# Kernel tuning notes

Hardware: AMD Instinct MI355X
Metric: run time of the kernel (lower is better)

## Reference

```python
import jax, jax.numpy as jnp
import numpy as np

Q_DIM, T_DIM, TOP_M, TEMP = 512, 768, 5, 0.07
B, H, W, K = 8, 64, 64, 128
LN_EPS = 1e-5

def _layernorm(x, g, b):
    mu = jnp.mean(x, axis=-1, keepdims=True)
    var = jnp.mean(jnp.square(x - mu), axis=-1, keepdims=True)
    return (x - mu) * jax.lax.rsqrt(var + LN_EPS) * g + b

def _l2norm(x):
    n = jnp.linalg.norm(x, axis=-1, keepdims=True)
    return x / jnp.maximum(n, 1e-12)

def setup_inputs() -> dict:
    key = jax.random.key(0)
    ks = jax.random.split(key, 12)
    s = lambda d: 1.0 / np.sqrt(d)
    return {
        'visual_features': jax.random.normal(ks[0], (B, H, W, Q_DIM), jnp.float32),
        'text_features': jax.random.normal(ks[1], (B, K, T_DIM), jnp.float32),
        'Wq': jax.random.uniform(ks[2], (Q_DIM, T_DIM), jnp.float32, -s(Q_DIM), s(Q_DIM)),
        'bq': jnp.zeros((T_DIM,), jnp.float32),
        'Wv': jax.random.uniform(ks[3], (T_DIM, Q_DIM), jnp.float32, -s(T_DIM), s(T_DIM)),
        'bv': jnp.zeros((Q_DIM,), jnp.float32),
        'W1': jax.random.uniform(ks[4], (Q_DIM, 4 * Q_DIM), jnp.float32, -s(Q_DIM), s(Q_DIM)),
        'b1': jnp.zeros((4 * Q_DIM,), jnp.float32),
        'W2': jax.random.uniform(ks[5], (4 * Q_DIM, Q_DIM), jnp.float32, -s(4 * Q_DIM), s(4 * Q_DIM)),
        'b2': jnp.zeros((Q_DIM,), jnp.float32),
        'g1': jnp.ones((Q_DIM,), jnp.float32), 'be1': jnp.zeros((Q_DIM,), jnp.float32),
        'g2': jnp.ones((Q_DIM,), jnp.float32), 'be2': jnp.zeros((Q_DIM,), jnp.float32),
    }

def reference(visual_features, text_features, Wq, bq, Wv, bv, W1, b1, W2, b2, g1, be1, g2, be2):
    b, h, w, c = visual_features.shape
    residual = visual_features.reshape(b, h * w, c)
    vis = _layernorm(residual, g1, be1)                      # (B,N,C)
    query = _l2norm(vis @ Wq + bq)                            # (B,N,Ct)
    keyt = _l2norm(text_features)                             # (B,K,Ct)
    value = text_features @ Wv + bv                           # (B,K,C)
    sim = jnp.einsum('bnc,bkc->bnk', query, keyt)             # (B,N,K)
    # top-M sparsification: keep top_m logits, others -> -inf
    top_v = jax.lax.top_k(sim, TOP_M)[0]                      # (B,N,M) sorted desc
    thr = top_v[..., -1:]
    sim = jnp.where(sim >= thr, sim, -jnp.inf)
    attn = jax.nn.softmax(sim / TEMP, axis=-1)
    aligned = jnp.einsum('bnk,bkc->bnc', attn, value)
    fused = residual + aligned
    fused = _layernorm(fused, g2, be2)
    ffn = jax.nn.gelu(fused @ W1 + b1, approximate=False) @ W2 + b2
    out = fused + ffn
    return out.reshape(b, h, w, c)
```

## Files before the change

kernel.cpp:

```cpp
#include <hip/hip_runtime.h>
#include <math.h>

typedef unsigned short u16;
typedef unsigned int   u32;
typedef unsigned long long u64;
typedef __attribute__((ext_vector_type(4))) float f32x4;
typedef __attribute__((ext_vector_type(4))) unsigned int u32x4;
typedef __attribute__((ext_vector_type(8))) _Float16 f16x8;
typedef __attribute__((ext_vector_type(8))) short s16x8;

#define NROWS   32768
#define CDIM    512
#define TDIM    768
#define KKEY    128
#define FFDIM   2048
#define NB      8
#define RPB     4096
#define LN_EPS_ 1e-5f
#define TINV    (1.0f/0.07f)
#define RESCUE_MARGIN 1e-5f

__device__ __forceinline__ u16 f2h(float f){ _Float16 h=(_Float16)f; return __builtin_bit_cast(u16,h); }
__device__ __forceinline__ float h2f(u16 v){ return (float)__builtin_bit_cast(_Float16, v); }
__device__ __forceinline__ unsigned pk2(float a,float b){ return (unsigned)f2h(a)|((unsigned)f2h(b)<<16); }
__device__ __forceinline__ u16 f2b(float f){
  u32 u = __builtin_bit_cast(u32, f);
  u32 r = (u + 0x7fffu + ((u>>16)&1u)) >> 16;
  return (u16)r;
}
__device__ __forceinline__ float b2f(u16 h){ u32 u = ((u32)h)<<16; return __builtin_bit_cast(float, u); }
__device__ __forceinline__ unsigned pkb(float a,float b){ return (unsigned)f2b(a)|((unsigned)f2b(b)<<16); }

__device__ __forceinline__ void gl_lds16(const void* g, void* l){
  __builtin_amdgcn_global_load_lds(
      (const __attribute__((address_space(1))) u32*)g,
      (__attribute__((address_space(3))) u32*)l, 16, 0, 0);
}

__device__ __forceinline__ float fast_exp2(float x){
#if __has_builtin(__builtin_amdgcn_exp2f)
  return __builtin_amdgcn_exp2f(x);
#else
  return exp2f(x);
#endif
}
__device__ __forceinline__ float fast_rcp(float x){
#if __has_builtin(__builtin_amdgcn_rcpf)
  return __builtin_amdgcn_rcpf(x);
#else
  return 1.0f/x;
#endif
}

__device__ __forceinline__ float wsumf(float v){
#pragma unroll
  for(int o=1;o<64;o<<=1) v+=__shfl_xor(v,o);
  return v; }
__device__ __forceinline__ float wmaxf(float v){
#pragma unroll
  for(int o=1;o<64;o<<=1) v=fmaxf(v,__shfl_xor(v,o));
  return v; }
__device__ __forceinline__ double wsumd(double v){
#pragma unroll
  for(int o=1;o<64;o<<=1) v+=__shfl_xor(v,o);
  return v; }
__device__ __forceinline__ double wmaxd(double v){
#pragma unroll
  for(int o=1;o<64;o<<=1){ double t=__shfl_xor(v,o); v = t>v ? t : v; }
  return v; }

__device__ __forceinline__ double blocksumd4(double v, double* red){
  const int lane = threadIdx.x & 63, w = threadIdx.x >> 6;
  v = wsumd(v);
  __syncthreads();
  if (lane==0) red[w] = v;
  __syncthreads();
  return red[0]+red[1]+red[2]+red[3];
}

template<int R, int C, int MODE>
__device__ __forceinline__ void tr_tile(const float* __restrict__ in, void* __restrict__ out,
                                        int bx, int by, float (*tile)[33])
{
  int c0 = bx*32, r0 = by*32;
  int tx = threadIdx.x, ty = threadIdx.y;
#pragma unroll
  for (int i=0;i<4;i++){
    int r = r0 + ty + i*8;
    tile[ty+i*8][tx] = in[(size_t)r*C + c0 + tx];
  }
  __syncthreads();
#pragma unroll
  for (int i=0;i<4;i++){
    int cc = c0 + ty + i*8, rr = r0 + tx;
    float v = tile[tx][ty+i*8];
    if (MODE==1)      ((u16*)out)[(size_t)cc*R + rr] = f2h(v);
    else if (MODE==2) ((u16*)out)[(size_t)cc*R + rr] = f2b(v);
    else              ((float*)out)[(size_t)cc*R + rr] = v;
  }
}

__global__ __launch_bounds__(256) void transpose_all_kernel(
    const float* __restrict__ Wq, const float* __restrict__ W1,
    const float* __restrict__ W2, const float* __restrict__ Wv,
    u16* __restrict__ Wqbt, u16* __restrict__ W116t,
    u16* __restrict__ W216t, float* __restrict__ WvT)
{
  __shared__ float tile[32][33];
  int bid = blockIdx.x;
  if (bid < 384){
    tr_tile<512,768,2>(Wq, Wqbt, bid%24, bid/24, tile);
  } else if (bid < 1408){
    int b = bid-384;  tr_tile<512,2048,1>(W1, W116t, b%64, b/64, tile);
  } else if (bid < 2432){
    int b = bid-1408; tr_tile<2048,512,1>(W2, W216t, b%16, b/16, tile);
  } else {
    int b = bid-2432; tr_tile<768,512,0>(Wv, WvT, b%16, b/16, tile);
  }
}

__global__ __launch_bounds__(256) void keystats_kernel(
    const float* __restrict__ text, const float* __restrict__ bq,
    float* __restrict__ normk, float* __restrict__ crr)
{
  int gw = blockIdx.x*4 + (threadIdx.x>>6);
  int lane = threadIdx.x & 63;
  const float* tr = &text[(size_t)gw*TDIM];
  double ss=0.0, db=0.0;
#pragma unroll
  for (int i=0;i<12;i++){
    float v = tr[lane + 64*i];
    ss += (double)v*(double)v;
    db += (double)bq[lane+64*i]*(double)v;
  }
  ss = wsumd(ss); db = wsumd(db);
  if (lane==0){
    double nk = sqrt(ss); nk = nk>1e-12 ? nk : 1e-12;
    normk[gw] = (float)nk;
    crr[gw]   = (float)db;
  }
}

__global__ __launch_bounds__(256) void ln1_kernel(
    const float* __restrict__ visual, const float* __restrict__ g1, const float* __restrict__ be1,
    u16* __restrict__ visH, u16* __restrict__ visL)
{
  int row = blockIdx.x*4 + (threadIdx.x>>6);
  int lane = threadIdx.x & 63;
  size_t base = (size_t)row*CDIM + lane*8;
  f32x4 a = *(const f32x4*)&visual[base];
  f32x4 c = *(const f32x4*)&visual[base+4];
  float s = a[0]+a[1]+a[2]+a[3]+c[0]+c[1]+c[2]+c[3];
  s = wsumf(s);
  float mu = s * (1.0f/512.0f);
  float q = 0.f;
#pragma unroll
  for (int i=0;i<4;i++){ float d=a[i]-mu; q+=d*d; }
#pragma unroll
  for (int i=0;i<4;i++){ float d=c[i]-mu; q+=d*d; }
  q = wsumf(q);
  float rs = rsqrtf(q*(1.0f/512.0f) + LN_EPS_);
  int cb = lane*8;
  float o[8];
#pragma unroll
  for (int i=0;i<4;i++) o[i]   = (a[i]-mu)*rs*g1[cb+i]   + be1[cb+i];
#pragma unroll
  for (int i=0;i<4;i++) o[4+i] = (c[i]-mu)*rs*g1[cb+4+i] + be1[cb+4+i];
  u16 hh[8];
  float lo[8];
#pragma unroll
  for (int i=0;i<8;i++){ hh[i] = f2b(o[i]); lo[i] = o[i] - b2f(hh[i]); }
  u32x4 hv, lv;
#pragma unroll
  for (int i=0;i<4;i++){
    hv[i] = (u32)hh[2*i] | ((u32)hh[2*i+1]<<16);
    lv[i] = pkb(lo[2*i], lo[2*i+1]);
  }
  *(u32x4*)&visH[base] = hv;
  *(u32x4*)&visL[base] = lv;
}

__global__ __launch_bounds__(256) void gemm_txt_kernel(
    const float* __restrict__ text, const float* __restrict__ Wq,
    const float* __restrict__ WvT,
    u16* __restrict__ MrtH, u16* __restrict__ MrtL, float* __restrict__ value)
{
  __shared__ float As[64][17];
  __shared__ float Bs[64][17];
  const int zz = blockIdx.z;
  const bool isV = zz >= 8;
  const int z = isV ? zz-8 : zz;
  const float* A  = text + (size_t)z*KKEY*TDIM;
  const float* Bt = isV ? WvT : Wq;
  const int tid = threadIdx.x;
  const int tx = tid & 15, ty = tid >> 4;
  const int m0 = blockIdx.x*64, n0 = blockIdx.y*64;
  float acc[4][4];
#pragma unroll
  for (int i=0;i<4;i++)
#pragma unroll
    for (int j=0;j<4;j++) acc[i][j]=0.f;
  const int lr = tid >> 2, lc = (tid & 3)*4;
  for (int k0=0; k0<TDIM; k0+=16){
    f32x4 av = *(const f32x4*)&A [(size_t)(m0+lr)*TDIM + k0 + lc];
    f32x4 bv = *(const f32x4*)&Bt[(size_t)(n0+lr)*TDIM + k0 + lc];
#pragma unroll
    for (int i=0;i<4;i++){ As[lr][lc+i]=av[i]; Bs[lr][lc+i]=bv[i]; }
    __syncthreads();
#pragma unroll
    for (int kk=0; kk<16; kk++){
      float a[4], b[4];
#pragma unroll
      for (int i=0;i<4;i++){ a[i]=As[ty*4+i][kk]; b[i]=Bs[tx*4+i][kk]; }
#pragma unroll
      for (int i=0;i<4;i++)
#pragma unroll
        for (int j=0;j<4;j++) acc[i][j] = fmaf(a[i], b[j], acc[i][j]);
    }
    __syncthreads();
  }
#pragma unroll
  for (int i=0;i<4;i++){
    size_t idx = ((size_t)z*KKEY + m0 + ty*4 + i)*CDIM + n0 + tx*4;
    if (isV){
      f32x4 o;
#pragma unroll
      for (int j=0;j<4;j++) o[j]=acc[i][j];
      *(f32x4*)&value[idx] = o;
    } else {
      u16 hh[4]; u16 ll[4];
#pragma unroll
      for (int j=0;j<4;j++){
        float v = acc[i][j];
        u16 h = f2b(v);
        hh[j] = h;
        ll[j] = f2b(v - b2f(h));
      }
      ((u32*)&MrtH[idx])[0] = (u32)hh[0] | ((u32)hh[1]<<16);
      ((u32*)&MrtH[idx])[1] = (u32)hh[2] | ((u32)hh[3]<<16);
      ((u32*)&MrtL[idx])[0] = (u32)ll[0] | ((u32)ll[1]<<16);
      ((u32*)&MrtL[idx])[1] = (u32)ll[2] | ((u32)ll[3]<<16);
    }
  }
}

__device__ __forceinline__ float gelu_exact(float v){
  float x  = v*0.70710678118654752440f;
  float ax = fabsf(x);
  float t  = fast_rcp(fmaf(0.3275911f, ax, 1.0f));
  float p  = t*fmaf(t, fmaf(t, fmaf(t, fmaf(t, 1.061405429f, -1.453152027f),
                  1.421413741f), -0.284496736f), 0.254829592f);
  float e  = fast_exp2(ax*ax*(-1.4426950408889634f));
  float y  = 1.0f - p*e;
  float er = (x < 0.0f) ? -y : y;
  return 0.5f*v*(1.0f + er);
}

template<int EPI, int NN, int KK, int NT, int TPB>
__global__ __launch_bounds__(256) void gemm_f16_kernel(
    const u16* __restrict__ A, const u16* __restrict__ Bt,
    const float* __restrict__ bias,
    float* __restrict__ out_f,
    u16* __restrict__ out_h,
    const u16* __restrict__ add_h)
{
  __shared__ __align__(16) u16 As[2][128*64];
  __shared__ __align__(16) u16 Bs[2][128*64];
  constexpr int KSTEPS = KK/64;
  constexpr int BPM = NT/TPB;
  constexpr int NWG = 256*BPM;
  constexpr int GTOT = TPB*KSTEPS;
  const int tid = threadIdx.x;
  const int lane = tid & 63, w = tid >> 6;
  const int wr = w >> 1, wc = w & 1;
  const int wg = blockIdx.x;
  const int b2 = (wg & 7)*(NWG/8) + (wg >> 3);
  const int mtile = b2 / BPM, nb = (b2 % BPM)*TPB;
  const int m0 = mtile*128;
  f32x4 acc[4][4];
#pragma unroll
  for (int i=0;i<4;i++)
#pragma unroll
    for (int j=0;j<4;j++) acc[i][j] = (f32x4)0.f;
  const int lr = lane & 15, lk = (lane >> 4)*8;
  const int c8_sw = ((lane & 7) ^ (lane >> 3))*8;
  const size_t stride32 = (size_t)32*KK;
  const int rowoff = w*8 + (lane>>3);
  const u16* aBase = &A [(size_t)(m0 + rowoff)*KK + c8_sw];
  const u16* bBase = &Bt[(size_t)(nb*128 + rowoff)*KK + c8_sw];

  auto STAGE = [&](int g, int buf){
    const int t = g / KSTEPS, k0 = (g & (KSTEPS-1))*64;
    const u16* ap = aBase + k0;
    const u16* bp = bBase + (size_t)t*128*KK + k0;
#pragma unroll
    for (int i=0;i<4;i++){
      gl_lds16(ap + i*stride32, &As[buf][w*512 + i*2048]);
      gl_lds16(bp + i*stride32, &Bs[buf][w*512 + i*2048]);
    }
  };

  const int lr4 = (lane >> 4)*4;
  STAGE(0, 0);
  for (int g=0; g<GTOT; ++g){
    const int cur = g & 1;
    if (g+1 < GTOT){
      STAGE(g+1, cur^1);
      asm volatile("s_waitcnt vmcnt(8)" ::: "memory");
    } else {
      asm volatile("s_waitcnt vmcnt(0)" ::: "memory");
    }
    __builtin_amdgcn_s_barrier();
#pragma unroll
    for (int kk=0; kk<64; kk+=32){
      s16x8 af[4], bfv[4];
      const int csw = (kk + lk) ^ ((lr & 7) << 3);
#pragma unroll
      for (int mi=0;mi<4;mi++) af[mi]  = *(const s16x8*)&As[cur][(wr*64 + mi*16 + lr)*64 + csw];
#pragma unroll
      for (int ni=0;ni<4;ni++) bfv[ni] = *(const s16x8*)&Bs[cur][(wc*64 + ni*16 + lr)*64 + csw];
#pragma unroll
      for (int mi=0;mi<4;mi++)
#pragma unroll
        for (int ni=0;ni<4;ni++){
          if (EPI == 0)
            acc[mi][ni] = __builtin_amdgcn_mfma_f32_16x16x32_bf16(af[mi], bfv[ni], acc[mi][ni], 0, 0, 0);
          else
            acc[mi][ni] = __builtin_amdgcn_mfma_f32_16x16x32_f16(
                __builtin_bit_cast(f16x8, af[mi]), __builtin_bit_cast(f16x8, bfv[ni]), acc[mi][ni], 0, 0, 0);
        }
    }
    __builtin_amdgcn_s_barrier();
    if ((g & (KSTEPS-1)) == KSTEPS-1){
      const int ntile = nb + g/KSTEPS;
      const int n0 = ntile*128;
      if (EPI == 0){
        float sq[4][4];
#pragma unroll
        for (int mi=0;mi<4;mi++)
#pragma unroll
          for (int r=0;r<4;r++) sq[mi][r]=0.f;
#pragma unroll
        for (int ni=0;ni<4;ni++){
          float bqv = bias[n0 + wc*64 + ni*16 + lr];
#pragma unroll
          for (int mi=0;mi<4;mi++)
#pragma unroll
            for (int r=0;r<4;r++){
              float v = acc[mi][ni][r] + bqv;
              sq[mi][r] += v*v;
            }
        }
#pragma unroll
        for (int o=1;o<16;o<<=1)
#pragma unroll
          for (int mi=0;mi<4;mi++)
#pragma unroll
            for (int r=0;r<4;r++) sq[mi][r] += __shfl_xor(sq[mi][r], o);
        if ((lane & 15) == 0){
          int part = ntile*2 + wc;
#pragma unroll
          for (int mi=0;mi<4;mi++)
#pragma unroll
            for (int r=0;r<4;r++){
              int row = m0 + wr*64 + mi*16 + lr4 + r;
              out_f[(size_t)row*12 + part] = sq[mi][r];
            }
        }
      } else {
        const int row0 = m0 + wr*64 + lr4;
        const int col0 = n0 + wc*64 + lr;
        float bb[4];
#pragma unroll
        for (int ni=0;ni<4;ni++) bb[ni] = bias[col0 + ni*16];
        if (EPI == 1){
          u16* op = out_h + (size_t)row0*NN + col0;
#pragma unroll
          for (int mi=0;mi<4;mi++)
#pragma unroll
            for (int r=0;r<4;r++)
#pragma unroll
              for (int ni=0;ni<4;ni++)
                op[(size_t)(mi*16+r)*NN + ni*16] = f2h(gelu_exact(acc[mi][ni][r] + bb[ni]));
        } else {
          float* op = out_f + (size_t)row0*NN + col0;
          const u16* rp = add_h + (size_t)row0*NN + col0;
#pragma unroll
          for (int mi=0;mi<4;mi++)
#pragma unroll
            for (int r=0;r<4;r++)
#pragma unroll
              for (int ni=0;ni<4;ni++)
                op[(size_t)(mi*16+r)*NN + ni*16] =
                    acc[mi][ni][r] + bb[ni] + h2f(rp[(size_t)(mi*16+r)*NN + ni*16]);
        }
      }
#pragma unroll
      for (int i=0;i<4;i++)
#pragma unroll
        for (int j=0;j<4;j++) acc[i][j] = (f32x4)0.f;
    }
  }
}

__global__ __launch_bounds__(256) void gemm_t_kernel(
    const u16* __restrict__ Ah, const u16* __restrict__ Al,
    const u16* __restrict__ Bh, const u16* __restrict__ Bl,
    float* __restrict__ C)
{
  __shared__ __align__(16) u16 As[2][128*64];
  __shared__ __align__(16) u16 Bs[2][128*64];
  const int tid = threadIdx.x;
  const int lane = tid & 63, w = tid >> 6;
  const int wr = w >> 1, wc = w & 1;
  const int wg = blockIdx.x;
  const int mtile = (wg & 7)*32 + (wg >> 3);
  const int m0 = mtile*128, z = mtile >> 5;
  f32x4 acc[4][4];
#pragma unroll
  for (int i=0;i<4;i++)
#pragma unroll
    for (int j=0;j<4;j++) acc[i][j] = (f32x4)0.f;
  const int lr = lane & 15, lk = (lane >> 4)*8;
  const int c8_sw = ((lane & 7) ^ (lane >> 3))*8;
  const int rowoff = w*8 + (lane>>3);
  const size_t aOff = (size_t)(m0 + rowoff)*CDIM + c8_sw;
  const size_t bOff = (size_t)(z*KKEY + rowoff)*CDIM + c8_sw;
  const size_t stride32 = (size_t)32*CDIM;

  auto STAGE = [&](int g, int buf){
    const int p = g >> 3, k0 = (g & 7) << 6;
    const u16* Ap = (p==2) ? Al : Ah;
    const u16* Bp = (p==1) ? Bl : Bh;
#pragma unroll
    for (int i=0;i<4;i++){
      gl_lds16(Ap + aOff + i*stride32 + k0, &As[buf][w*512 + i*2048]);
      gl_lds16(Bp + bOff + i*stride32 + k0, &Bs[buf][w*512 + i*2048]);
    }
  };

  STAGE(0, 0);
  for (int g=0; g<24; ++g){
    const int cur = g & 1;
    if (g < 23){
      STAGE(g+1, cur^1);
      asm volatile("s_waitcnt vmcnt(8)" ::: "memory");
    } else {
      asm volatile("s_waitcnt vmcnt(0)" ::: "memory");
    }
    __builtin_amdgcn_s_barrier();
#pragma unroll
    for (int kk=0; kk<64; kk+=32){
      s16x8 af[4], bfv[4];
      const int csw = (kk + lk) ^ ((lr & 7) << 3);
#pragma unroll
      for (int mi=0;mi<4;mi++) af[mi]  = *(const s16x8*)&As[cur][(wr*64 + mi*16 + lr)*64 + csw];
#pragma unroll
      for (int ni=0;ni<4;ni++) bfv[ni] = *(const s16x8*)&Bs[cur][(wc*64 + ni*16 + lr)*64 + csw];
#pragma unroll
      for (int mi=0;mi<4;mi++)
#pragma unroll
        for (int ni=0;ni<4;ni++)
          acc[mi][ni] = __builtin_amdgcn_mfma_f32_16x16x32_bf16(af[mi], bfv[ni], acc[mi][ni], 0, 0, 0);
    }
    __builtin_amdgcn_s_barrier();
  }
  const int lr4 = (lane >> 4)*4;
  const int row0 = m0 + wr*64 + lr4;
  const int col0 = wc*64 + lr;
  float* op = C + (size_t)row0*KKEY + col0;
#pragma unroll
  for (int mi=0;mi<4;mi++)
#pragma unroll
    for (int r=0;r<4;r++)
#pragma unroll
      for (int ni=0;ni<4;ni++)
        op[(size_t)(mi*16+r)*KKEY + ni*16] = acc[mi][ni][r];
}

__global__ __launch_bounds__(256) void rescue_kernel(
    const int* __restrict__ rcnt, const int* __restrict__ rlist,
    const float* __restrict__ visual, const float* __restrict__ text,
    const float* __restrict__ Wq, const float* __restrict__ bq,
    const float* __restrict__ g1, const float* __restrict__ be1,
    const float* __restrict__ g2, const float* __restrict__ be2,
    const float* __restrict__ value, const float* __restrict__ bv,
    u16* __restrict__ fused16)
{
  __shared__ double vis64[512];
  __shared__ double q64[768];
  __shared__ double sims[128];
  __shared__ double pw[128];
  __shared__ double red[4];
  __shared__ double sc2[2];
  __shared__ int klist[128];
  __shared__ int kcount;
  const int tid = threadIdx.x, lane = tid & 63, w = tid >> 6;
  int n = *rcnt; if (n > NROWS) n = NROWS;
  for (int i = blockIdx.x; i < n; i += gridDim.x){
    const int row = rlist[i], b = row >> 12;
    const size_t rb = (size_t)row*CDIM;
    double x0 = (double)visual[rb+tid], x1 = (double)visual[rb+tid+256];
    double s = blocksumd4(x0+x1, red);
    double mu = s*(1.0/512.0);
    double d0 = x0-mu, d1 = x1-mu;
    double var = blocksumd4(d0*d0+d1*d1, red);
    double rs = 1.0/sqrt(var*(1.0/512.0) + 1e-5);
    vis64[tid]     = d0*rs*(double)g1[tid]     + (double)be1[tid];
    vis64[tid+256] = d1*rs*(double)g1[tid+256] + (double)be1[tid+256];
    __syncthreads();
    double qa0=(double)bq[tid], qa1=(double)bq[tid+256], qa2=(double)bq[tid+512];
#pragma unroll 4
    for (int c=0;c<CDIM;c++){
      double v = vis64[c];
      const float* wrow = &Wq[(size_t)c*TDIM];
      qa0 += v*(double)wrow[tid];
      qa1 += v*(double)wrow[tid+256];
      qa2 += v*(double)wrow[tid+512];
    }
    q64[tid]=qa0; q64[tid+256]=qa1; q64[tid+512]=qa2;
    double nq2 = blocksumd4(qa0*qa0+qa1*qa1+qa2*qa2, red);
    double nq = sqrt(nq2); if (nq < 1e-12) nq = 1e-12;
    __syncthreads();
    if (tid < KKEY){
      const float* trow = &text[((size_t)b*KKEY + tid)*TDIM];
      double dot=0.0, nk2=0.0;
#pragma unroll 8
      for (int j=0;j<TDIM;j++){
        double tv = (double)trow[j];
        dot += q64[j]*tv; nk2 += tv*tv;
      }
      double nk = sqrt(nk2); if (nk < 1e-12) nk = 1e-12;
      sims[tid] = dot/(nq*nk);
    }
    __syncthreads();
    if (w == 0){
      double v0=sims[lane], v1=sims[lane+64];
      bool rm0=false, rm1=false;
      double thr=0.0, smax=0.0;
      for (int it=0; it<5; ++it){
        double c0 = rm0 ? -1e300 : v0;
        double c1 = rm1 ? -1e300 : v1;
        double m = wmaxd(c0>c1 ? c0 : c1);
        if (it==0) smax = m;
        thr = m;
        bool h0 = (!rm0) && (v0==m);
        u64 k0 = __ballot(h0);
        if (k0){ if (lane == __ffsll(k0)-1) rm0 = true; }
        else {
          bool h1 = (!rm1) && (v1==m);
          u64 k1 = __ballot(h1);
          if (lane == __ffsll(k1)-1) rm1 = true;
        }
      }
      if (lane==0){ sc2[0]=smax; sc2[1]=thr; kcount=0; }
    }
    __syncthreads();
    const double smax = sc2[0], thr = sc2[1];
    double p = 0.0;
    if (tid < KKEY){
      double sv = sims[tid];
      p = (sv >= thr) ? exp((sv-smax)*(1.0/0.07)) : 0.0;
      pw[tid] = p;
      if (p > 0.0){ int pos = atomicAdd(&kcount, 1); klist[pos] = tid; }
    }
    double Z = blocksumd4(p, red);
    double zi = 1.0/Z;
    __syncthreads();
    double a0=(double)bv[tid], a1=(double)bv[tid+256];
    int kc = kcount;
    for (int ki=0; ki<kc; ++ki){
      int k = klist[ki];
      double wt = pw[k]*zi;
      const float* vr = &value[((size_t)b*KKEY + k)*CDIM];
      a0 += wt*(double)vr[tid];
      a1 += wt*(double)vr[tid+256];
    }
    double f0 = (double)visual[rb+tid]     + a0;
    double f1 = (double)visual[rb+tid+256] + a1;
    double fsum = blocksumd4(f0+f1, red);
    double fmu = fsum*(1.0/512.0);
    double e0=f0-fmu, e1=f1-fmu;
    double fvar = blocksumd4(e0*e0+e1*e1, red);
    double frs = 1.0/sqrt(fvar*(1.0/512.0) + 1e-5);
    fused16[rb+tid]     = f2h((float)(e0*frs*(double)g2[tid]     + (double)be2[tid]));
    fused16[rb+tid+256] = f2h((float)(e1*frs*(double)g2[tid+256] + (double)be2[tid+256]));
    __syncthreads();
  }
}

__global__ __launch_bounds__(256) void attn_ln2_kernel(
    const float* __restrict__ visual,
    const float* __restrict__ tbuf, const float* __restrict__ crr,
    const float* __restrict__ normk, const float* __restrict__ qpart,
    const float* __restrict__ value, const float* __restrict__ bv,
    const float* __restrict__ g2, const float* __restrict__ be2,
    u16* __restrict__ fused16,
    int* __restrict__ rcnt, int* __restrict__ rlist)
{
  const int w = threadIdx.x >> 6, lane = threadIdx.x & 63;
  const int row = blockIdx.x*4 + w;
  const int b = row >> 12;
  float nqp = (lane < 12) ? qpart[(size_t)row*12 + lane] : 0.f;
  float nq2 = wsumf(nqp);
  float nq = fmaxf(sqrtf(nq2), 1e-12f);
  const float* trow = &tbuf[(size_t)row*KKEY];
  float s0 = (trow[lane]    + crr[b*KKEY + lane])    / (nq*normk[b*KKEY + lane]);
  float s1 = (trow[lane+64] + crr[b*KKEY + lane+64]) / (nq*normk[b*KKEY + lane+64]);
  float v0=s0, v1=s1; bool rm0=false, rm1=false;
  float thr=0.f, smax=0.f, m6=0.f;
  for (int it=0; it<6; ++it){
    float c0 = rm0 ? -1e30f : v0;
    float c1 = rm1 ? -1e30f : v1;
    float m = wmaxf(fmaxf(c0,c1));
    if (it==0) smax = m;
    if (it<5){
      thr = m;
      bool h0 = (!rm0) && (v0==m);
      u64 k0 = __ballot(h0);
      if (k0){ if (lane == __ffsll(k0)-1) rm0 = true; }
      else {
        bool h1 = (!rm1) && (v1==m);
        u64 k1 = __ballot(h1);
        if (lane == __ffsll(k1)-1) rm1 = true;
      }
    } else m6 = m;
  }
  if ((thr - m6) < RESCUE_MARGIN){
    if (lane == 0){
      int p = atomicAdd(rcnt, 1);
      rlist[p] = row;
    }
    return;
  }
  float p0 = (s0>=thr) ? expf((s0-smax)*TINV) : 0.f;
  float p1 = (s1>=thr) ? expf((s1-smax)*TINV) : 0.f;
  float Z = wsumf(p0+p1);
  float zi = 1.f/Z;
  float accv[8];
#pragma unroll
  for (int j=0;j<8;j++) accv[j] = bv[lane*8+j];
  u64 mk0 = __ballot(p0>0.f);
  u64 mk1 = __ballot(p1>0.f);
  while (mk0){
    int l = __ffsll(mk0)-1; mk0 &= mk0-1;
    float wt = __shfl(p0, l)*zi;
    const f32x4* vr = (const f32x4*)&value[((size_t)b*KKEY + l)*CDIM + lane*8];
    f32x4 va = vr[0], vb = vr[1];
#pragma unroll
    for (int j=0;j<4;j++){ accv[j] += wt*va[j]; accv[4+j] += wt*vb[j]; }
  }
  while (mk1){
    int l = __ffsll(mk1)-1; mk1 &= mk1-1;
    float wt = __shfl(p1, l)*zi;
    const f32x4* vr = (const f32x4*)&value[((size_t)b*KKEY + l + 64)*CDIM + lane*8];
    f32x4 va = vr[0], vb = vr[1];
#pragma unroll
    for (int j=0;j<4;j++){ accv[j] += wt*va[j]; accv[4+j] += wt*vb[j]; }
  }
  size_t rb = (size_t)row*CDIM + lane*8;
  f32x4 r0v = *(const f32x4*)&visual[rb];
  f32x4 r1v = *(const f32x4*)&visual[rb+4];
  float f[8];
#pragma unroll
  for (int j=0;j<4;j++){ f[j]=r0v[j]+accv[j]; f[4+j]=r1v[j]+accv[4+j]; }
  float fs=0.f;
#pragma unroll
  for (int j=0;j<8;j++) fs += f[j];
  fs = wsumf(fs);
  float fmu = fs*(1.0f/512.0f);
  float fvv=0.f;
#pragma unroll
  for (int j=0;j<8;j++){ float d=f[j]-fmu; fvv+=d*d; }
  fvv = wsumf(fvv);
  float frs = rsqrtf(fvv*(1.0f/512.0f) + LN_EPS_);
  int cb = lane*8;
  f32x4 o0,o1;
#pragma unroll
  for (int j=0;j<4;j++) o0[j] = (f[j]-fmu)*frs*g2[cb+j]     + be2[cb+j];
#pragma unroll
  for (int j=0;j<4;j++) o1[j] = (f[4+j]-fmu)*frs*g2[cb+4+j] + be2[cb+4+j];
  u32x4 hv;
  hv[0]=pk2(o0[0],o0[1]); hv[1]=pk2(o0[2],o0[3]);
  hv[2]=pk2(o1[0],o1[1]); hv[3]=pk2(o1[2],o1[3]);
  *(u32x4*)&fused16[rb] = hv;
}

extern "C" void kernel_launch(void* const* d_in, const int* in_sizes, int n_in,
                              void* d_out, int out_size, void* d_ws, size_t ws_size,
                              hipStream_t stream)
{
  (void)in_sizes; (void)n_in; (void)out_size; (void)ws_size;
  const float* visual = (const float*)d_in[0];
  const float* text   = (const float*)d_in[1];
  const float* Wq     = (const float*)d_in[2];
  const float* bq     = (const float*)d_in[3];
  const float* Wv     = (const float*)d_in[4];
  const float* bv     = (const float*)d_in[5];
  const float* W1     = (const float*)d_in[6];
  const float* b1     = (const float*)d_in[7];
  const float* W2     = (const float*)d_in[8];
  const float* b2     = (const float*)d_in[9];
  const float* g1     = (const float*)d_in[10];
  const float* be1    = (const float*)d_in[11];
  const float* g2     = (const float*)d_in[12];
  const float* be2    = (const float*)d_in[13];
  float* out = (float*)d_out;

  char* ws = (char*)d_ws;
  size_t off = 0;
  auto alloc = [&](size_t bytes)->char*{
    char* p = ws + off; off += (bytes + 255) & ~(size_t)255; return p; };

  u16*    visH   = (u16*)   alloc((size_t)NROWS*CDIM*2);
  u16*    visL   = (u16*)   alloc((size_t)NROWS*CDIM*2);
  u16*    h16    = (u16*)   alloc((size_t)NROWS*FFDIM*2);
  u16*    fused16= (u16*)   alloc((size_t)NROWS*CDIM*2);
  u16*    MrtH   = (u16*)   alloc((size_t)NB*KKEY*CDIM*2);
  u16*    MrtL   = (u16*)   alloc((size_t)NB*KKEY*CDIM*2);
  float*  value  = (float*) alloc((size_t)NB*KKEY*CDIM*4);
  u16*    Wqbt   = (u16*)   alloc((size_t)TDIM*CDIM*2);
  u16*    W116t  = (u16*)   alloc((size_t)FFDIM*CDIM*2);
  u16*    W216t  = (u16*)   alloc((size_t)CDIM*FFDIM*2);
  float*  WvT    = (float*) alloc((size_t)CDIM*TDIM*4);
  float*  qpart  = (float*) alloc((size_t)NROWS*12*4);
  float*  normk  = (float*) alloc((size_t)NB*KKEY*4);
  float*  crr    = (float*) alloc((size_t)NB*KKEY*4);
  int*    rcnt   = (int*)   alloc(256);
  int*    rlist  = (int*)   alloc((size_t)NROWS*4);
  float*  tbuf   = (float*)h16;

  hipMemsetAsync(rcnt, 0, sizeof(int), stream);

  transpose_all_kernel<<<2816, dim3(32,8), 0, stream>>>(
      Wq, W1, W2, Wv, Wqbt, W116t, W216t, WvT);
  keystats_kernel<<<256, 256, 0, stream>>>(text, bq, normk, crr);
  gemm_txt_kernel<<<dim3(2, 8, 16), 256, 0, stream>>>(
      text, Wq, WvT, MrtH, MrtL, value);
  ln1_kernel<<<NROWS/4, 256, 0, stream>>>(visual, g1, be1, visH, visL);
  gemm_t_kernel<<<256, 256, 0, stream>>>(visH, visL, MrtH, MrtL, tbuf);
  gemm_f16_kernel<0,TDIM,CDIM,6,3><<<512, 256, 0, stream>>>(
      visH, Wqbt, bq, qpart, nullptr, nullptr);
  attn_ln2_kernel<<<NROWS/4, 256, 0, stream>>>(
      visual, tbuf, crr, normk, qpart, value, bv, g2, be2,
      fused16, rcnt, rlist);
  rescue_kernel<<<256, 256, 0, stream>>>(
      rcnt, rlist, visual, text, Wq, bq, g1, be1, g2, be2, value, bv, fused16);
  gemm_f16_kernel<1,FFDIM,CDIM,16,8><<<512, 256, 0, stream>>>(
      fused16, W116t, b1, nullptr, h16, nullptr);
  gemm_f16_kernel<2,CDIM,FFDIM,4,2><<<512, 256, 0, stream>>>(
      h16, W216t, b2, out, nullptr, fused16);
}
```

Before: 504.6 us.

## Reorder GEMM work so each block keeps one B tile and walks M tiles

The persistent f16 GEMM now gives each workgroup a fixed N tile and a chain of M tiles, instead of a fixed M tile sweeping several N tiles. The B (weight) tile stays the same across the chain, so repeated weight reads mostly hit cache, while A rows stream through. Launch configurations change accordingly: the Q-norm GEMM uses 384 blocks with chains of 4, and the FFN1 GEMM uses 1024 blocks with chains of 4. The trade-off is that A activations are no longer reused across N tiles within a block, and the grid sizes and wave counts change.

Result: slower. 517.2 us (+2.5%).

```diff
diff --git a/kernel.cpp b/kernel.cpp
--- a/kernel.cpp
+++ b/kernel.cpp
@@ -266,17 +266,15 @@
 {
   __shared__ __align__(16) u16 As[2][128*64];
   __shared__ __align__(16) u16 Bs[2][128*64];
-  constexpr int KSTEPS = KK/64;
-  constexpr int BPM = NT/TPB;
-  constexpr int NWG = 256*BPM;
-  constexpr int GTOT = TPB*KSTEPS;
+  constexpr int MCH = 256/TPB;
+  constexpr int NWG = MCH*NT;
   const int tid = threadIdx.x;
   const int lane = tid & 63, w = tid >> 6;
   const int wr = w >> 1, wc = w & 1;
   const int wg = blockIdx.x;
   const int b2 = (wg & 7)*(NWG/8) + (wg >> 3);
-  const int mtile = b2 / BPM, nb = (b2 % BPM)*TPB;
-  const int m0 = mtile*128;
+  const int mchain = b2 / NT, ntile = b2 % NT;
+  const int n0 = ntile*128;
   f32x4 acc[4][4];
 #pragma unroll
   for (int i=0;i<4;i++)
@@ -285,121 +283,123 @@
   const int lr = lane & 15, lk = (lane >> 4)*8;
   const int c8_sw = ((lane & 7) ^ (lane >> 3))*8;
   const size_t stride32 = (size_t)32*KK;
+  const size_t TSTRIDE  = (size_t)128*KK;
   const int rowoff = w*8 + (lane>>3);
-  const u16* aBase = &A [(size_t)(m0 + rowoff)*KK + c8_sw];
-  const u16* bBase = &Bt[(size_t)(nb*128 + rowoff)*KK + c8_sw];
-
-  auto STAGE = [&](int g, int buf){
-    const int t = g / KSTEPS, k0 = (g & (KSTEPS-1))*64;
-    const u16* ap = aBase + k0;
-    const u16* bp = bBase + (size_t)t*128*KK + k0;
+  const u16* aBase0 = &A [(size_t)(mchain*TPB*128 + rowoff)*KK + c8_sw];
+  const u16* bBase  = &Bt[(size_t)(n0 + rowoff)*KK + c8_sw];
+
+  auto STAGE = [&](const u16* ap, int k0, int buf){
 #pragma unroll
     for (int i=0;i<4;i++){
-      gl_lds16(ap + i*stride32, &As[buf][w*512 + i*2048]);
-      gl_lds16(bp + i*stride32, &Bs[buf][w*512 + i*2048]);
+      gl_lds16(ap    + i*stride32 + k0, &As[buf][w*512 + i*2048]);
+      gl_lds16(bBase + i*stride32 + k0, &Bs[buf][w*512 + i*2048]);
     }
   };
 
   const int lr4 = (lane >> 4)*4;
-  STAGE(0, 0);
-  for (int g=0; g<GTOT; ++g){
-    const int cur = g & 1;
-    if (g+1 < GTOT){
-      STAGE(g+1, cur^1);
-      asm volatile("s_waitcnt vmcnt(8)" ::: "memory");
+  int cur = 0;
+  STAGE(aBase0, 0, 0);
+  for (int t=0; t<TPB; ++t){
+    const u16* aT = aBase0 + (size_t)t*TSTRIDE;
+    for (int k0=0; k0<KK; k0+=64){
+      if (k0 + 64 < KK){
+        STAGE(aT, k0+64, cur^1);
+        asm volatile("s_waitcnt vmcnt(8)" ::: "memory");
+      } else if (t+1 < TPB){
+        STAGE(aT + TSTRIDE, 0, cur^1);
+        asm volatile("s_waitcnt vmcnt(8)" ::: "memory");
+      } else {
+        asm volatile("s_waitcnt vmcnt(0)" ::: "memory");
+      }
+      __builtin_amdgcn_s_barrier();
+#pragma unroll
+      for (int kk=0; kk<64; kk+=32){
+        s16x8 af[4], bfv[4];
+        const int csw = (kk + lk) ^ ((lr & 7) << 3);
+#pragma unroll
+        for (int mi=0;mi<4;mi++) af[mi]  = *(const s16x8*)&As[cur][(wr*64 + mi*16 + lr)*64 + csw];
+#pragma unroll
+        for (int ni=0;ni<4;ni++) bfv[ni] = *(const s16x8*)&Bs[cur][(wc*64 + ni*16 + lr)*64 + csw];
+#pragma unroll
+        for (int mi=0;mi<4;mi++)
+#pragma unroll
+          for (int ni=0;ni<4;ni++){
+            if (EPI == 0)
+              acc[mi][ni] = __builtin_amdgcn_mfma_f32_16x16x32_bf16(af[mi], bfv[ni], acc[mi][ni], 0, 0, 0);
+            else
+              acc[mi][ni] = __builtin_amdgcn_mfma_f32_16x16x32_f16(
+                  __builtin_bit_cast(f16x8, af[mi]), __builtin_bit_cast(f16x8, bfv[ni]), acc[mi][ni], 0, 0, 0);
+          }
+      }
+      __builtin_amdgcn_s_barrier();
+      cur ^= 1;
+    }
+    const int m0 = (mchain*TPB + t)*128;
+    if (EPI == 0){
+      float sq[4][4];
+#pragma unroll
+      for (int mi=0;mi<4;mi++)
+#pragma unroll
+        for (int r=0;r<4;r++) sq[mi][r]=0.f;
+#pragma unroll
+      for (int ni=0;ni<4;ni++){
+        float bqv = bias[n0 + wc*64 + ni*16 + lr];
+#pragma unroll
+        for (int mi=0;mi<4;mi++)
+#pragma unroll
+          for (int r=0;r<4;r++){
+            float v = acc[mi][ni][r] + bqv;
+            sq[mi][r] += v*v;
+          }
+      }
+#pragma unroll
+      for (int o=1;o<16;o<<=1)
+#pragma unroll
+        for (int mi=0;mi<4;mi++)
+#pragma unroll
+          for (int r=0;r<4;r++) sq[mi][r] += __shfl_xor(sq[mi][r], o);
+      if ((lane & 15) == 0){
+        int part = ntile*2 + wc;
+#pragma unroll
+        for (int mi=0;mi<4;mi++)
+#pragma unroll
+          for (int r=0;r<4;r++){
+            int row = m0 + wr*64 + mi*16 + lr4 + r;
+            out_f[(size_t)row*12 + part] = sq[mi][r];
+          }
+      }
     } else {
-      asm volatile("s_waitcnt vmcnt(0)" ::: "memory");
-    }
-    __builtin_amdgcn_s_barrier();
-#pragma unroll
-    for (int kk=0; kk<64; kk+=32){
-      s16x8 af[4], bfv[4];
-      const int csw = (kk + lk) ^ ((lr & 7) << 3);
-#pragma unroll
-      for (int mi=0;mi<4;mi++) af[mi]  = *(const s16x8*)&As[cur][(wr*64 + mi*16 + lr)*64 + csw];
-#pragma unroll
-      for (int ni=0;ni<4;ni++) bfv[ni] = *(const s16x8*)&Bs[cur][(wc*64 + ni*16 + lr)*64 + csw];
-#pragma unroll
-      for (int mi=0;mi<4;mi++)
-#pragma unroll
-        for (int ni=0;ni<4;ni++){
-          if (EPI == 0)
-            acc[mi][ni] = __builtin_amdgcn_mfma_f32_16x16x32_bf16(af[mi], bfv[ni], acc[mi][ni], 0, 0, 0);
-          else
-            acc[mi][ni] = __builtin_amdgcn_mfma_f32_16x16x32_f16(
-                __builtin_bit_cast(f16x8, af[mi]), __builtin_bit_cast(f16x8, bfv[ni]), acc[mi][ni], 0, 0, 0);
-        }
-    }
-    __builtin_amdgcn_s_barrier();
-    if ((g & (KSTEPS-1)) == KSTEPS-1){
-      const int ntile = nb + g/KSTEPS;
-      const int n0 = ntile*128;
-      if (EPI == 0){
-        float sq[4][4];
+      const int row0 = m0 + wr*64 + lr4;
+      const int col0 = n0 + wc*64 + lr;
+      float bb[4];
+#pragma unroll
+      for (int ni=0;ni<4;ni++) bb[ni] = bias[col0 + ni*16];
+      if (EPI == 1){
+        u16* op = out_h + (size_t)row0*NN + col0;
 #pragma unroll
         for (int mi=0;mi<4;mi++)
 #pragma unroll
-          for (int r=0;r<4;r++) sq[mi][r]=0.f;
-#pragma unroll
-        for (int ni=0;ni<4;ni++){
-          float bqv = bias[n0 + wc*64 + ni*16 + lr];
-#pragma unroll
-          for (int mi=0;mi<4;mi++)
-#pragma unroll
-            for (int r=0;r<4;r++){
-              float v = acc[mi][ni][r] + bqv;
-              sq[mi][r] += v*v;
-            }
-        }
-#pragma unroll
-        for (int o=1;o<16;o<<=1)
-#pragma unroll
-          for (int mi=0;mi<4;mi++)
-#pragma unroll
-            for (int r=0;r<4;r++) sq[mi][r] += __shfl_xor(sq[mi][r], o);
-        if ((lane & 15) == 0){
-          int part = ntile*2 + wc;
-#pragma unroll
-          for (int mi=0;mi<4;mi++)
-#pragma unroll
-            for (int r=0;r<4;r++){
-              int row = m0 + wr*64 + mi*16 + lr4 + r;
-              out_f[(size_t)row*12 + part] = sq[mi][r];
-            }
-        }
+          for (int r=0;r<4;r++)
+#pragma unroll
+            for (int ni=0;ni<4;ni++)
+              op[(size_t)(mi*16+r)*NN + ni*16] = f2h(gelu_exact(acc[mi][ni][r] + bb[ni]));
       } else {
-        const int row0 = m0 + wr*64 + lr4;
-        const int col0 = n0 + wc*64 + lr;
-        float bb[4];
-#pragma unroll
-        for (int ni=0;ni<4;ni++) bb[ni] = bias[col0 + ni*16];
-        if (EPI == 1){
-          u16* op = out_h + (size_t)row0*NN + col0;
-#pragma unroll
-          for (int mi=0;mi<4;mi++)
-#pragma unroll
-            for (int r=0;r<4;r++)
-#pragma unroll
-              for (int ni=0;ni<4;ni++)
-                op[(size_t)(mi*16+r)*NN + ni*16] = f2h(gelu_exact(acc[mi][ni][r] + bb[ni]));
-        } else {
-          float* op = out_f + (size_t)row0*NN + col0;
-          const u16* rp = add_h + (size_t)row0*NN + col0;
-#pragma unroll
-          for (int mi=0;mi<4;mi++)
-#pragma unroll
-            for (int r=0;r<4;r++)
-#pragma unroll
-              for (int ni=0;ni<4;ni++)
-                op[(size_t)(mi*16+r)*NN + ni*16] =
-                    acc[mi][ni][r] + bb[ni] + h2f(rp[(size_t)(mi*16+r)*NN + ni*16]);
-        }
-      }
-#pragma unroll
-      for (int i=0;i<4;i++)
-#pragma unroll
-        for (int j=0;j<4;j++) acc[i][j] = (f32x4)0.f;
-    }
+        float* op = out_f + (size_t)row0*NN + col0;
+        const u16* rp = add_h + (size_t)row0*NN + col0;
+#pragma unroll
+        for (int mi=0;mi<4;mi++)
+#pragma unroll
+          for (int r=0;r<4;r++)
+#pragma unroll
+            for (int ni=0;ni<4;ni++)
+              op[(size_t)(mi*16+r)*NN + ni*16] =
+                  acc[mi][ni][r] + bb[ni] + h2f(rp[(size_t)(mi*16+r)*NN + ni*16]);
+      }
+    }
+#pragma unroll
+    for (int i=0;i<4;i++)
+#pragma unroll
+      for (int j=0;j<4;j++) acc[i][j] = (f32x4)0.f;
   }
 }
 
@@ -739,14 +739,14 @@
       text, Wq, WvT, MrtH, MrtL, value);
   ln1_kernel<<<NROWS/4, 256, 0, stream>>>(visual, g1, be1, visH, visL);
   gemm_t_kernel<<<256, 256, 0, stream>>>(visH, visL, MrtH, MrtL, tbuf);
-  gemm_f16_kernel<0,TDIM,CDIM,6,3><<<512, 256, 0, stream>>>(
+  gemm_f16_kernel<0,TDIM,CDIM,6,4><<<384, 256, 0, stream>>>(
       visH, Wqbt, bq, qpart, nullptr, nullptr);
   attn_ln2_kernel<<<NROWS/4, 256, 0, stream>>>(
       visual, tbuf, crr, normk, qpart, value, bv, g2, be2,
       fused16, rcnt, rlist);
   rescue_kernel<<<256, 256, 0, stream>>>(
       rcnt, rlist, visual, text, Wq, bq, g1, be1, g2, be2, value, bv, fused16);
-  gemm_f16_kernel<1,FFDIM,CDIM,16,8><<<512, 256, 0, stream>>>(
+  gemm_f16_kernel<1,FFDIM,CDIM,16,4><<<1024, 256, 0, stream>>>(
       fused16, W116t, b1, nullptr, h16, nullptr);
   gemm_f16_kernel<2,CDIM,FFDIM,4,2><<<512, 256, 0, stream>>>(
       h16, W216t, b2, out, nullptr, fused16);
```
